# Performance work log

Hardware: AMD Instinct MI355X
Metric: run time of the kernel (lower is better)

The kernel has to match this reference:

```python
import jax, jax.numpy as jnp
import numpy as np

N = 100000   # nodes
E = 3200000  # edges
G = 1024     # graphs in the batch
H = 64       # hidden_dim


def setup_inputs() -> dict:
    key = jax.random.key(0)
    ks = jax.random.split(key, 12)
    x = jax.random.normal(ks[0], (N, 1), dtype=jnp.float32)
    edge_index = jax.random.randint(ks[1], (2, E), 0, N, dtype=jnp.int32)
    batch = jnp.sort(jax.random.randint(ks[2], (N,), 0, G, dtype=jnp.int32))
    s = 0.1
    w1 = jax.random.normal(ks[3], (1, H), dtype=jnp.float32) * s
    b1 = jnp.zeros((H,), dtype=jnp.float32)
    w2 = jax.random.normal(ks[4], (H, H), dtype=jnp.float32) * s
    b2 = jnp.zeros((H,), dtype=jnp.float32)
    w3 = jax.random.normal(ks[5], (H, H), dtype=jnp.float32) * s
    b3 = jnp.zeros((H,), dtype=jnp.float32)
    fc_w = jax.random.normal(ks[6], (H, 1), dtype=jnp.float32) * s
    fc_b = jnp.zeros((1,), dtype=jnp.float32)
    return {"x": x, "edge_index": edge_index, "batch": batch,
            "w1": w1, "b1": b1, "w2": w2, "b2": b2, "w3": w3, "b3": b3,
            "fc_w": fc_w, "fc_b": fc_b}


def _gcn_norm(edge_index, n):
    # add self-loops: A_hat = A + I
    src = jnp.concatenate([edge_index[0], jnp.arange(n, dtype=edge_index.dtype)])
    dst = jnp.concatenate([edge_index[1], jnp.arange(n, dtype=edge_index.dtype)])
    deg = jax.ops.segment_sum(jnp.ones_like(dst, dtype=jnp.float32), dst, num_segments=n)
    dinv = jnp.where(deg > 0, jax.lax.rsqrt(deg), 0.0)
    norm = dinv[src] * dinv[dst]  # [E+N]
    return src, dst, norm


def _gcn_conv(x, w, b, src, dst, norm, n):
    h = x @ w                               # [N, H] transform first (PyG order)
    msg = h[src] * norm[:, None]            # gather + scale  [E+N, H]
    out = jax.ops.segment_sum(msg, dst, num_segments=n)  # scatter-add
    return out + b


def reference(x, edge_index, batch, w1, b1, w2, b2, w3, b3, fc_w, fc_b):
    n = x.shape[0]
    src, dst, norm = _gcn_norm(edge_index, n)
    h = jax.nn.relu(_gcn_conv(x, w1, b1, src, dst, norm, n))
    h = jax.nn.relu(_gcn_conv(h, w2, b2, src, dst, norm, n))
    h = jax.nn.relu(_gcn_conv(h, w3, b3, src, dst, norm, n))
    # global mean pool over graphs
    sums = jax.ops.segment_sum(h, batch, num_segments=G)                 # [G, H]
    cnts = jax.ops.segment_sum(jnp.ones((n,), jnp.float32), batch, num_segments=G)
    pooled = sums / jnp.maximum(cnts, 1.0)[:, None]
    return pooled @ fc_w + fc_b  # [G, 1]
```

## Files before the change

kernel.cpp:

```cpp
#include <hip/hip_runtime.h>
#include <hip/hip_bf16.h>


#define WS_ALIGN(x) (((x) + 255) & ~size_t(255))
#define NCHUNK 8
#define CSH 14
#define NB 32
#define RPW (NB / 4)
#define NBIN (NB * NCHUNK)
#define USH 17
#define UMASK 0x1FFFF
#define BKTMAX 256
#define SBS 512
#define SBKEYS (SBS * NCHUNK)
#define P1T 2048

__device__ __forceinline__ float bf2f(unsigned short h) {
    union { unsigned u; float f; } t;
    t.u = ((unsigned)h) << 16;
    return t.f;
}
__device__ __forceinline__ unsigned short f2bf(float f) {
    union { float f; unsigned u; } t;
    t.f = f;
    unsigned r = t.u + 0x7FFF + ((t.u >> 16) & 1);
    return (unsigned short)(r >> 16);
}
__device__ __forceinline__ float bfLo(unsigned v) {
    union { unsigned u; float f; } t;
    t.u = v << 16;
    return t.f;
}
__device__ __forceinline__ float bfHi(unsigned v) {
    union { unsigned u; float f; } t;
    t.u = v & 0xFFFF0000u;
    return t.f;
}

__global__ __launch_bounds__(256) void k_zero(int g, int e, int* bucketCnt,
                                              int* gCursor, int* csr,
                                              float* gsum, float* gcnt) {
    int i = blockIdx.x * blockDim.x + threadIdx.x;
    if (i < BKTMAX) { bucketCnt[i] = 0; gCursor[i] = 0; }
    if (i < g) { gsum[i] = 0.f; gcnt[i] = 0.f; }
    if (i < 4) csr[e + i] = 0;
}

__global__ __launch_bounds__(256) void k_cnt1(int e, const int* __restrict__ dst,
                                              int* __restrict__ bucketCnt) {
    __shared__ int c[BKTMAX];
    int tid = threadIdx.x;
    c[tid] = 0;
    __syncthreads();
    int base = blockIdx.x * P1T;
#pragma unroll
    for (int q = 0; q < P1T / 256; ++q) {
        int i = base + q * 256 + tid;
        if (i < e) atomicAdd(&c[dst[i] >> 9], 1);
    }
    __syncthreads();
    if (c[tid] > 0) atomicAdd(&bucketCnt[tid], c[tid]);
}

__global__ __launch_bounds__(256) void k_scanB(int nbkt, int e,
                                               const int* __restrict__ bucketCnt,
                                               int* __restrict__ bucketStart) {
    __shared__ int sd[256];
    int tid = threadIdx.x;
    int v = (tid < nbkt) ? bucketCnt[tid] : 0;
    sd[tid] = v;
    __syncthreads();
    for (int off = 1; off < 256; off <<= 1) {
        int t = (tid >= off) ? sd[tid - off] : 0;
        __syncthreads();
        sd[tid] += t;
        __syncthreads();
    }
    if (tid < nbkt) bucketStart[tid] = sd[tid] - v;
    if (tid == 0) bucketStart[nbkt] = e;
}

__global__ __launch_bounds__(256) void k_p1(int e, const int* __restrict__ src,
                                            const int* __restrict__ dst,
                                            const int* __restrict__ bucketStart,
                                            int* __restrict__ gCursor,
                                            int* __restrict__ pkbuf) {
    __shared__ int cnt[BKTMAX], exc[BKTMAX], cur[BKTMAX], bb[BKTMAX];
    __shared__ int sd[256];
    __shared__ int stage[P1T];
    __shared__ unsigned char stgb[P1T];
    int tid = threadIdx.x;
    cnt[tid] = 0;
    __syncthreads();
    int base = blockIdx.x * P1T;
    int m = e - base; if (m > P1T) m = P1T;
    int pk8[P1T / 256];
    int b8[P1T / 256];
#pragma unroll
    for (int q = 0; q < P1T / 256; ++q) {
        int li = q * 256 + tid;
        if (li < m) {
            int d = dst[base + li];
            int s = src[base + li];
            int b = d >> 9;
            b8[q] = b;
            pk8[q] = ((d & (SBS - 1)) << USH) | s;
            atomicAdd(&cnt[b], 1);
        }
    }
    __syncthreads();
    int cv = cnt[tid];
    sd[tid] = cv;
    __syncthreads();
    for (int off = 1; off < 256; off <<= 1) {
        int t = (tid >= off) ? sd[tid - off] : 0;
        __syncthreads();
        sd[tid] += t;
        __syncthreads();
    }
    exc[tid] = sd[tid] - cv;
    cur[tid] = sd[tid] - cv;
    if (cv > 0) bb[tid] = atomicAdd(&gCursor[tid], cv);
    __syncthreads();
#pragma unroll
    for (int q = 0; q < P1T / 256; ++q) {
        int li = q * 256 + tid;
        if (li < m) {
            int b = b8[q];
            int pos = atomicAdd(&cur[b], 1);
            stage[pos] = pk8[q];
            stgb[pos] = (unsigned char)b;
        }
    }
    __syncthreads();
#pragma unroll
    for (int q = 0; q < P1T / 256; ++q) {
        int p = q * 256 + tid;
        if (p < m) {
            int b = stgb[p];
            pkbuf[bucketStart[b] + bb[b] + (p - exc[b])] = stage[p];
        }
    }
}

__global__ __launch_bounds__(256) void k_p2(int n, const int* __restrict__ bucketStart,
                                            const int* __restrict__ pkbuf,
                                            const float* __restrict__ x,
                                            int* __restrict__ csr,
                                            int* __restrict__ boundsG,
                                            float* __restrict__ dinv,
                                            float* __restrict__ xs) {
    __shared__ int cnt[SBKEYS + 1];
    __shared__ int sd[256];
    int sb = blockIdx.x, tid = threadIdx.x;
    int r0 = bucketStart[sb], r1 = bucketStart[sb + 1];
    for (int k = tid; k < SBKEYS + 1; k += 256) cnt[k] = 0;
    __syncthreads();
    for (int i = r0 + tid; i < r1; i += 256) {
        int w = pkbuf[i];
        int key = ((w >> USH) << 3) | ((w & UMASK) >> CSH);
        atomicAdd(&cnt[key], 1);
    }
    __syncthreads();
    int base16 = tid * 16;
    int loc[16]; int s = 0;
#pragma unroll
    for (int j = 0; j < 16; ++j) { loc[j] = cnt[base16 + j]; s += loc[j]; }
    sd[tid] = s;
    __syncthreads();
    for (int off = 1; off < 256; off <<= 1) {
        int t = (tid >= off) ? sd[tid - off] : 0;
        __syncthreads();
        sd[tid] += t;
        __syncthreads();
    }
    int run = sd[tid] - s;
#pragma unroll
    for (int j = 0; j < 16; ++j) { cnt[base16 + j] = run; run += loc[j]; }
    if (tid == 255) cnt[SBKEYS] = run;
    __syncthreads();
    for (int k = tid; k < SBKEYS; k += 256) {
        int bi = sb * 16 + (k >> 8);
        boundsG[(size_t)bi * (NBIN + 1) + (k & 255)] = r0 + cnt[k];
    }
    if (tid < 16)
        boundsG[(size_t)(sb * 16 + tid) * (NBIN + 1) + NBIN] = r0 + cnt[(tid + 1) * 256];
    for (int dl = tid; dl < SBS; dl += 256) {
        int v = sb * SBS + dl;
        if (v < n) {
            int deg = cnt[dl * 8 + 8] - cnt[dl * 8] + 1;
            float di = 1.0f / sqrtf((float)deg);
            dinv[v] = di;
            xs[v] = x[v] * di;
        }
    }
    __syncthreads();
    for (int i = r0 + tid; i < r1; i += 256) {
        int w = pkbuf[i];
        int srcv = w & UMASK;
        int key = ((w >> USH) << 3) | (srcv >> CSH);
        int pos = atomicAdd(&cnt[key], 1);
        csr[r0 + pos] = srcv;
    }
}

__global__ __launch_bounds__(256, 8) void k_layer1(int n, const int* __restrict__ boundsG,
                                                   const int* __restrict__ csr,
                                                   const float* __restrict__ xs,
                                                   const float* __restrict__ dinv,
                                                   const float* __restrict__ w1,
                                                   const float* __restrict__ b1,
                                                   unsigned short* __restrict__ hs_out) {
    int tid = threadIdx.x;
    int r = tid >> 6, lane = tid & 63;
    float w1r = w1[lane], b1r = b1[lane];
    int wid = blockIdx.x * 4 + r;
    int stride = gridDim.x * 4;
    for (int v = wid; v < n; v += stride) {
        int bi = v / NB, vi = v & (NB - 1);
        size_t base = (size_t)bi * (NBIN + 1) + vi * NCHUNK;
        int s0 = boundsG[base], s1 = boundsG[base + NCHUNK];
        float acc = 0.f;
        for (int k = s0 + lane; k < s1; k += 64) acc += xs[csr[k]];
#pragma unroll
        for (int m = 32; m > 0; m >>= 1) acc += __shfl_xor(acc, m, 64);
        float dv = dinv[v];
        float s = (acc + xs[v]) * dv;
        hs_out[(size_t)v * 64 + lane] = f2bf(fmaxf(s * w1r + b1r, 0.f) * dv);
    }
}

#define GATHER_CORE                                                            \
    __shared__ float ws[64 * 64];                                              \
    __shared__ float rowl[4][64];                                              \
    __shared__ int bndL[NBIN + 1];                                             \
    int tid = threadIdx.x;                                                     \
    int lane = tid & 63;                                                       \
    int r = tid >> 6;                                                          \
    int h = lane >> 5;                                                         \
    int fi = lane & 31;                                                        \
    int v0 = blockIdx.x * NB;                                                  \
    const unsigned* hsu = (const unsigned*)hs_in;                              \
    for (int k = tid; k < 64 * 64; k += 256) ws[k] = w[k];                     \
    for (int i = tid; i < NBIN + 1; i += 256)                                  \
        bndL[i] = boundsG[(size_t)blockIdx.x * (NBIN + 1) + i];                \
    float accLo[RPW], accHi[RPW];                                              \
    _Pragma("unroll")                                                          \
    for (int q = 0; q < RPW; ++q) {                                            \
        int v = v0 + q * 4 + r;                                                \
        unsigned sv = (v < n && h == 0) ? hsu[(size_t)v * 32 + fi] : 0u;       \
        accLo[q] = bfLo(sv);                                                   \
        accHi[q] = bfHi(sv);                                                   \
    }                                                                          \
    __syncthreads();                                                           \
    _Pragma("unroll")                                                          \
    for (int t = 0; t < RPW / 2; ++t) {                                        \
        int viA = (2 * t) * 4 + r;                                             \
        int viB = (2 * t + 1) * 4 + r;                                         \
        int ba = __builtin_amdgcn_readfirstlane(bndL[viA * NCHUNK]);           \
        int a1 = __builtin_amdgcn_readfirstlane(bndL[viA * NCHUNK + NCHUNK]);  \
        int bb = __builtin_amdgcn_readfirstlane(bndL[viB * NCHUNK]);           \
        int b1_ = __builtin_amdgcn_readfirstlane(bndL[viB * NCHUNK + NCHUNK]); \
        int pa = (a1 - ba > 0) ? ba : bb;                                      \
        int pb = (b1_ - bb > 0) ? bb : ba;                                     \
                               \
        int uA0 = csr[pa], uA1 = csr[pa + 1], uA2 = csr[pa + 2], uA3 = csr[pa + 3]; \
        int uB0 = csr[pb], uB1 = csr[pb + 1], uB2 = csr[pb + 2], uB3 = csr[pb + 3]; \
        unsigned gA01 = hsu[(size_t)(h ? uA1 : uA0) * 32 + fi];                \
        unsigned gA23 = hsu[(size_t)(h ? uA3 : uA2) * 32 + fi];                \
        unsigned gB01 = hsu[(size_t)(h ? uB1 : uB0) * 32 + fi];                \
        unsigned gB23 = hsu[(size_t)(h ? uB3 : uB2) * 32 + fi];                \
        while (ba < a1 || bb < b1_) {                                          \
            int na = ba + 4, nb = bb + 4;                                      \
            int pa2 = (a1 - na > 0) ? na : ((b1_ - nb > 0) ? nb : pa);         \
            int pb2 = (b1_ - nb > 0) ? nb : ((a1 - na > 0) ? na : pb);         \
                                  \
            int vA0 = csr[pa2], vA1 = csr[pa2 + 1], vA2 = csr[pa2 + 2], vA3 = csr[pa2 + 3]; \
            int vB0 = csr[pb2], vB1 = csr[pb2 + 1], vB2 = csr[pb2 + 2], vB3 = csr[pb2 + 3]; \
            unsigned nA01 = hsu[(size_t)(h ? vA1 : vA0) * 32 + fi];            \
            unsigned nA23 = hsu[(size_t)(h ? vA3 : vA2) * 32 + fi];            \
            unsigned nB01 = hsu[(size_t)(h ? vB1 : vB0) * 32 + fi];            \
            unsigned nB23 = hsu[(size_t)(h ? vB3 : vB2) * 32 + fi];            \
                              \
            int remA = a1 - ba, remB = b1_ - bb;                               \
            float mA0 = (remA > h) ? 1.f : 0.f;                                \
            float mA1 = (remA > 2 + h) ? 1.f : 0.f;                            \
            float mB0 = (remB > h) ? 1.f : 0.f;                                \
            float mB1 = (remB > 2 + h) ? 1.f : 0.f;                            \
            accLo[2 * t]     += bfLo(gA01) * mA0 + bfLo(gA23) * mA1;           \
            accHi[2 * t]     += bfHi(gA01) * mA0 + bfHi(gA23) * mA1;           \
            accLo[2 * t + 1] += bfLo(gB01) * mB0 + bfLo(gB23) * mB1;           \
            accHi[2 * t + 1] += bfHi(gB01) * mB0 + bfHi(gB23) * mB1;           \
            gA01 = nA01; gA23 = nA23; gB01 = nB01; gB23 = nB23;                \
            pa = pa2; pb = pb2;                                                \
            ba = na; bb = nb;                                                  \
        }                                                                      \
    }

__global__ __launch_bounds__(256, 4) void k_gg_mid(int n,
                                                   const int* __restrict__ boundsG,
                                                   const int* __restrict__ csr,
                                                   const unsigned short* __restrict__ hs_in,
                                                   const float* __restrict__ dinv,
                                                   const float* __restrict__ w,
                                                   const float* __restrict__ b,
                                                   unsigned short* __restrict__ hs_out) {
    GATHER_CORE
    float breg = b[lane];
#pragma unroll 1
    for (int q = 0; q < RPW; ++q) {
        int v = v0 + q * 4 + r;
        if (v >= n) continue;
        float dv = dinv[v];
        float lo = accLo[q]; lo += __shfl_xor(lo, 32, 64);
        float hi = accHi[q]; hi += __shfl_xor(hi, 32, 64);
        if (h == 0) {
            rowl[r][2 * fi] = lo * dv;
            rowl[r][2 * fi + 1] = hi * dv;
        }
        float o = breg;
#pragma unroll
        for (int k = 0; k < 64; ++k) o += rowl[r][k] * ws[k * 64 + lane];
        hs_out[(size_t)v * 64 + lane] = f2bf(fmaxf(o, 0.f) * dv);
    }
}

__global__ __launch_bounds__(256, 4) void k_gg_final(int n,
                                                     const int* __restrict__ boundsG,
                                                     const int* __restrict__ csr,
                                                     const unsigned short* __restrict__ hs_in,
                                                     const float* __restrict__ dinv,
                                                     const float* __restrict__ w,
                                                     const float* __restrict__ b,
                                                     const float* __restrict__ fcw,
                                                     float* __restrict__ dots) {
    GATHER_CORE
    float breg = b[lane];
    float freg = fcw[lane];
#pragma unroll 1
    for (int q = 0; q < RPW; ++q) {
        int v = v0 + q * 4 + r;
        if (v >= n) continue;
        float dv = dinv[v];
        float lo = accLo[q]; lo += __shfl_xor(lo, 32, 64);
        float hi = accHi[q]; hi += __shfl_xor(hi, 32, 64);
        if (h == 0) {
            rowl[r][2 * fi] = lo * dv;
            rowl[r][2 * fi + 1] = hi * dv;
        }
        float o = breg;
#pragma unroll
        for (int k = 0; k < 64; ++k) o += rowl[r][k] * ws[k * 64 + lane];
        float val = fmaxf(o, 0.f) * freg;
#pragma unroll
        for (int m = 32; m > 0; m >>= 1) val += __shfl_xor(val, m, 64);
        if (lane == 0) dots[v] = val;
    }
}

__global__ __launch_bounds__(256) void k_pool(int n, const float* __restrict__ dots,
                                              const int* __restrict__ batch,
                                              float* __restrict__ gsum,
                                              float* __restrict__ gcnt) {
    __shared__ float ls[64], lc[64];
    __shared__ int gmin_s;
    int tid = threadIdx.x;
    int i0 = blockIdx.x * 1024;
    if (tid == 0) gmin_s = batch[i0];
    if (tid < 64) { ls[tid] = 0.f; lc[tid] = 0.f; }
    __syncthreads();
    int gmin = gmin_s;
#pragma unroll
    for (int c = 0; c < 4; ++c) {
        int i = i0 + c * 256 + tid;
        if (i < n) {
            int g = batch[i];
            float d = dots[i];
            int rr = g - gmin;
            if (rr < 64) {
                atomicAdd(&ls[rr], d);
                atomicAdd(&lc[rr], 1.f);
            } else {
                atomicAdd(&gsum[g], d);
                atomicAdd(&gcnt[g], 1.f);
            }
        }
    }
    __syncthreads();
    if (tid < 64 && lc[tid] != 0.f) {
        atomicAdd(&gsum[gmin + tid], ls[tid]);
        atomicAdd(&gcnt[gmin + tid], lc[tid]);
    }
}

__global__ __launch_bounds__(256) void k_out(int g, const float* __restrict__ gsum,
                                             const float* __restrict__ gcnt,
                                             const float* __restrict__ fcb,
                                             float* __restrict__ out) {
    int i = blockIdx.x * blockDim.x + threadIdx.x;
    if (i < g) out[i] = gsum[i] / fmaxf(gcnt[i], 1.f) + fcb[0];
}

extern "C" void kernel_launch(void* const* d_in, const int* in_sizes, int n_in,
                              void* d_out, int out_size, void* d_ws, size_t ws_size,
                              hipStream_t stream) {
    const float* x    = (const float*)d_in[0];
    const int*   ei   = (const int*)d_in[1];
    const int*   batch= (const int*)d_in[2];
    const float* w1   = (const float*)d_in[3];
    const float* b1   = (const float*)d_in[4];
    const float* w2   = (const float*)d_in[5];
    const float* b2   = (const float*)d_in[6];
    const float* w3   = (const float*)d_in[7];
    const float* b3   = (const float*)d_in[8];
    const float* fcw  = (const float*)d_in[9];
    const float* fcb  = (const float*)d_in[10];
    float* out = (float*)d_out;

    const int N = in_sizes[0];
    const int E = in_sizes[1] / 2;
    const int G = out_size;
    const int H = 64;
    const int nbkt = (N + SBS - 1) / SBS;
    const int NBLK = (N + NB - 1) / NB;
    const int NBLKP = nbkt * 16;

    const int* src = ei;
    const int* dst = ei + E;

    char* p = (char*)d_ws;
    int*   bucketCnt   = (int*)p; p += WS_ALIGN(sizeof(int) * BKTMAX);
    int*   bucketStart = (int*)p; p += WS_ALIGN(sizeof(int) * (BKTMAX + 1));
    int*   gCursor     = (int*)p; p += WS_ALIGN(sizeof(int) * BKTMAX);
    int*   pkbuf       = (int*)p; p += WS_ALIGN(sizeof(int) * (size_t)E);
    int*   csr         = (int*)p; p += WS_ALIGN(sizeof(int) * ((size_t)E + 4));
    int*   boundsG     = (int*)p; p += WS_ALIGN(sizeof(int) * (size_t)NBLKP * (NBIN + 1));
    float* dinv        = (float*)p; p += WS_ALIGN(sizeof(float) * N);
    float* xs          = (float*)p; p += WS_ALIGN(sizeof(float) * N);
    unsigned short* bufA = (unsigned short*)p; p += WS_ALIGN(sizeof(unsigned short) * (size_t)N * H);
    unsigned short* bufB = (unsigned short*)p; p += WS_ALIGN(sizeof(unsigned short) * (size_t)N * H);
    float* dots        = (float*)p; p += WS_ALIGN(sizeof(float) * N);
    float* gsum        = (float*)p; p += WS_ALIGN(sizeof(float) * G);
    float* gcnt        = (float*)p; p += WS_ALIGN(sizeof(float) * G);

    const int B = 256;
    int gridZ    = ((G > BKTMAX ? G : BKTMAX) + B - 1) / B;
    int gridT    = (E + P1T - 1) / P1T;
    int gridG    = (G + B - 1) / B;
    int gridPool = (N + 1023) / 1024;
    int gridPers = 2048;
    if (gridPers * 4 > N) gridPers = (N + 3) / 4;

    k_zero<<<gridZ, B, 0, stream>>>(G, E, bucketCnt, gCursor, csr, gsum, gcnt);
    k_cnt1<<<gridT, B, 0, stream>>>(E, dst, bucketCnt);
    k_scanB<<<1, B, 0, stream>>>(nbkt, E, bucketCnt, bucketStart);
    k_p1<<<gridT, B, 0, stream>>>(E, src, dst, bucketStart, gCursor, pkbuf);
    k_p2<<<nbkt, B, 0, stream>>>(N, bucketStart, pkbuf, x, csr, boundsG, dinv, xs);
    k_layer1<<<gridPers, B, 0, stream>>>(N, boundsG, csr, xs, dinv, w1, b1, bufA);
    k_gg_mid<<<NBLK, B, 0, stream>>>(N, boundsG, csr, bufA, dinv, w2, b2, bufB);
    k_gg_final<<<NBLK, B, 0, stream>>>(N, boundsG, csr, bufB, dinv, w3, b3, fcw, dots);
    k_pool<<<gridPool, B, 0, stream>>>(N, dots, batch, gsum, gcnt);
    k_out<<<gridG, B, 0, stream>>>(G, gsum, gcnt, fcb, out);
}
```

Before: 326.5 us.

## Pad CSR rows to multiples of four with a dummy zero node

New measurement: 327.2 us. Within noise of the previous version (+0.2%).

```diff
diff --git a/kernel.cpp b/kernel.cpp
--- a/kernel.cpp
+++ b/kernel.cpp
@@ -7,13 +7,13 @@
 #define CSH 14
 #define NB 32
 #define RPW (NB / 4)
-#define NBIN (NB * NCHUNK)
 #define USH 17
 #define UMASK 0x1FFFF
 #define BKTMAX 256
 #define SBS 512
 #define SBKEYS (SBS * NCHUNK)
 #define P1T 2048
+#define PADGAP 1540
 
 __device__ __forceinline__ float bf2f(unsigned short h) {
     union { unsigned u; float f; } t;
@@ -37,13 +37,19 @@
     return t.f;
 }
 
-__global__ __launch_bounds__(256) void k_zero(int g, int e, int* bucketCnt,
-                                              int* gCursor, int* csr,
+__global__ __launch_bounds__(256) void k_zero(int g, int n, int* bucketCnt,
+                                              int* gCursor, float* xs,
+                                              unsigned short* bufA,
+                                              unsigned short* bufB,
                                               float* gsum, float* gcnt) {
     int i = blockIdx.x * blockDim.x + threadIdx.x;
     if (i < BKTMAX) { bucketCnt[i] = 0; gCursor[i] = 0; }
     if (i < g) { gsum[i] = 0.f; gcnt[i] = 0.f; }
-    if (i < 4) csr[e + i] = 0;
+    if (i < 64) {
+        bufA[(size_t)n * 64 + i] = 0;
+        bufB[(size_t)n * 64 + i] = 0;
+    }
+    if (i == 0) xs[n] = 0.f;
 }
 
 __global__ __launch_bounds__(256) void k_cnt1(int e, const int* __restrict__ dst,
@@ -147,13 +153,16 @@
                                             const int* __restrict__ pkbuf,
                                             const float* __restrict__ x,
                                             int* __restrict__ csr,
-                                            int* __restrict__ boundsG,
+                                            int* __restrict__ bndRow,
                                             float* __restrict__ dinv,
                                             float* __restrict__ xs) {
     __shared__ int cnt[SBKEYS + 1];
     __shared__ int sd[256];
+    __shared__ int padOff[SBS];
+    __shared__ int padTotal_s;
     int sb = blockIdx.x, tid = threadIdx.x;
     int r0 = bucketStart[sb], r1 = bucketStart[sb + 1];
+    int r0pad = r0 + sb * PADGAP;
     for (int k = tid; k < SBKEYS + 1; k += 256) cnt[k] = 0;
     __syncthreads();
     for (int i = r0 + tid; i < r1; i += 256) {
@@ -179,32 +188,58 @@
     for (int j = 0; j < 16; ++j) { cnt[base16 + j] = run; run += loc[j]; }
     if (tid == 255) cnt[SBKEYS] = run;
     __syncthreads();
-    for (int k = tid; k < SBKEYS; k += 256) {
-        int bi = sb * 16 + (k >> 8);
-        boundsG[(size_t)bi * (NBIN + 1) + (k & 255)] = r0 + cnt[k];
-    }
-    if (tid < 16)
-        boundsG[(size_t)(sb * 16 + tid) * (NBIN + 1) + NBIN] = r0 + cnt[(tid + 1) * 256];
+    int d0 = tid * 2, d1 = tid * 2 + 1;
+    int len0 = cnt[d0 * 8 + 8] - cnt[d0 * 8];
+    int len1 = cnt[d1 * 8 + 8] - cnt[d1 * 8];
+    int p0 = (-len0) & 3, p1 = (-len1) & 3;
+    int tsum = p0 + p1;
+    sd[tid] = tsum;
+    __syncthreads();
+    for (int off = 1; off < 256; off <<= 1) {
+        int t = (tid >= off) ? sd[tid - off] : 0;
+        __syncthreads();
+        sd[tid] += t;
+        __syncthreads();
+    }
+    int pexcl = sd[tid] - tsum;
+    padOff[d0] = pexcl;
+    padOff[d1] = pexcl + p0;
+    if (tid == 255) padTotal_s = pexcl + tsum;
+    __syncthreads();
     for (int dl = tid; dl < SBS; dl += 256) {
+        int gbi = sb * 16 + (dl >> 5);
+        int vi = dl & 31;
+        int startp = r0pad + cnt[dl * 8] + padOff[dl];
+        bndRow[gbi * 33 + vi] = startp;
+        if (vi == 0 && dl > 0) bndRow[(gbi - 1) * 33 + 32] = startp;
         int v = sb * SBS + dl;
         if (v < n) {
-            int deg = cnt[dl * 8 + 8] - cnt[dl * 8] + 1;
-            float di = 1.0f / sqrtf((float)deg);
+            int len = cnt[dl * 8 + 8] - cnt[dl * 8];
+            float di = 1.0f / sqrtf((float)(len + 1));
             dinv[v] = di;
             xs[v] = x[v] * di;
         }
+        int padc = (-(cnt[dl * 8 + 8] - cnt[dl * 8])) & 3;
+        int ps = r0pad + cnt[dl * 8 + 8] + padOff[dl];
+        for (int j = 0; j < padc; ++j) csr[ps + j] = n;
+    }
+    if (tid == 0) {
+        int endp = r0pad + cnt[SBKEYS] + padTotal_s;
+        bndRow[(sb * 16 + 15) * 33 + 32] = endp;
+        csr[endp] = n; csr[endp + 1] = n; csr[endp + 2] = n; csr[endp + 3] = n;
     }
     __syncthreads();
     for (int i = r0 + tid; i < r1; i += 256) {
         int w = pkbuf[i];
         int srcv = w & UMASK;
-        int key = ((w >> USH) << 3) | (srcv >> CSH);
+        int dl = w >> USH;
+        int key = (dl << 3) | (srcv >> CSH);
         int pos = atomicAdd(&cnt[key], 1);
-        csr[r0 + pos] = srcv;
-    }
-}
-
-__global__ __launch_bounds__(256, 8) void k_layer1(int n, const int* __restrict__ boundsG,
+        csr[r0pad + pos + padOff[dl]] = srcv;
+    }
+}
+
+__global__ __launch_bounds__(256, 8) void k_layer1(int n, const int* __restrict__ bndRow,
                                                    const int* __restrict__ csr,
                                                    const float* __restrict__ xs,
                                                    const float* __restrict__ dinv,
@@ -217,9 +252,8 @@
     int wid = blockIdx.x * 4 + r;
     int stride = gridDim.x * 4;
     for (int v = wid; v < n; v += stride) {
-        int bi = v / NB, vi = v & (NB - 1);
-        size_t base = (size_t)bi * (NBIN + 1) + vi * NCHUNK;
-        int s0 = boundsG[base], s1 = boundsG[base + NCHUNK];
+        int bi = v >> 5, vi = v & 31;
+        int s0 = bndRow[bi * 33 + vi], s1 = bndRow[bi * 33 + vi + 1];
         float acc = 0.f;
         for (int k = s0 + lane; k < s1; k += 64) acc += xs[csr[k]];
 #pragma unroll
@@ -233,7 +267,7 @@
 #define GATHER_CORE                                                            \
     __shared__ float ws[64 * 64];                                              \
     __shared__ float rowl[4][64];                                              \
-    __shared__ int bndL[NBIN + 1];                                             \
+    __shared__ int bndL[NB + 1];                                               \
     int tid = threadIdx.x;                                                     \
     int lane = tid & 63;                                                       \
     int r = tid >> 6;                                                          \
@@ -242,8 +276,7 @@
     int v0 = blockIdx.x * NB;                                                  \
     const unsigned* hsu = (const unsigned*)hs_in;                              \
     for (int k = tid; k < 64 * 64; k += 256) ws[k] = w[k];                     \
-    for (int i = tid; i < NBIN + 1; i += 256)                                  \
-        bndL[i] = boundsG[(size_t)blockIdx.x * (NBIN + 1) + i];                \
+    if (tid < NB + 1) bndL[tid] = bndRow[blockIdx.x * 33 + tid];               \
     float accLo[RPW], accHi[RPW];                                              \
     _Pragma("unroll")                                                          \
     for (int q = 0; q < RPW; ++q) {                                            \
@@ -257,13 +290,12 @@
     for (int t = 0; t < RPW / 2; ++t) {                                        \
         int viA = (2 * t) * 4 + r;                                             \
         int viB = (2 * t + 1) * 4 + r;                                         \
-        int ba = __builtin_amdgcn_readfirstlane(bndL[viA * NCHUNK]);           \
-        int a1 = __builtin_amdgcn_readfirstlane(bndL[viA * NCHUNK + NCHUNK]);  \
-        int bb = __builtin_amdgcn_readfirstlane(bndL[viB * NCHUNK]);           \
-        int b1_ = __builtin_amdgcn_readfirstlane(bndL[viB * NCHUNK + NCHUNK]); \
-        int pa = (a1 - ba > 0) ? ba : bb;                                      \
-        int pb = (b1_ - bb > 0) ? bb : ba;                                     \
-                               \
+        int ba = __builtin_amdgcn_readfirstlane(bndL[viA]);                    \
+        int a1 = __builtin_amdgcn_readfirstlane(bndL[viA + 1]);                \
+        int bb = __builtin_amdgcn_readfirstlane(bndL[viB]);                    \
+        int b1_ = __builtin_amdgcn_readfirstlane(bndL[viB + 1]);               \
+        int pa = (ba < a1) ? ba : bb;                                          \
+        int pb = (bb < b1_) ? bb : ba;                                         \
         int uA0 = csr[pa], uA1 = csr[pa + 1], uA2 = csr[pa + 2], uA3 = csr[pa + 3]; \
         int uB0 = csr[pb], uB1 = csr[pb + 1], uB2 = csr[pb + 2], uB3 = csr[pb + 3]; \
         unsigned gA01 = hsu[(size_t)(h ? uA1 : uA0) * 32 + fi];                \
@@ -272,25 +304,21 @@
         unsigned gB23 = hsu[(size_t)(h ? uB3 : uB2) * 32 + fi];                \
         while (ba < a1 || bb < b1_) {                                          \
             int na = ba + 4, nb = bb + 4;                                      \
-            int pa2 = (a1 - na > 0) ? na : ((b1_ - nb > 0) ? nb : pa);         \
-            int pb2 = (b1_ - nb > 0) ? nb : ((a1 - na > 0) ? na : pb);         \
-                                  \
+            int pa2 = (na < a1) ? na : ((nb < b1_) ? nb : pa);                 \
+            int pb2 = (nb < b1_) ? nb : ((na < a1) ? na : pb);                 \
             int vA0 = csr[pa2], vA1 = csr[pa2 + 1], vA2 = csr[pa2 + 2], vA3 = csr[pa2 + 3]; \
             int vB0 = csr[pb2], vB1 = csr[pb2 + 1], vB2 = csr[pb2 + 2], vB3 = csr[pb2 + 3]; \
             unsigned nA01 = hsu[(size_t)(h ? vA1 : vA0) * 32 + fi];            \
             unsigned nA23 = hsu[(size_t)(h ? vA3 : vA2) * 32 + fi];            \
             unsigned nB01 = hsu[(size_t)(h ? vB1 : vB0) * 32 + fi];            \
             unsigned nB23 = hsu[(size_t)(h ? vB3 : vB2) * 32 + fi];            \
-                              \
-            int remA = a1 - ba, remB = b1_ - bb;                               \
-            float mA0 = (remA > h) ? 1.f : 0.f;                                \
-            float mA1 = (remA > 2 + h) ? 1.f : 0.f;                            \
-            float mB0 = (remB > h) ? 1.f : 0.f;                                \
-            float mB1 = (remB > 2 + h) ? 1.f : 0.f;                            \
-            accLo[2 * t]     += bfLo(gA01) * mA0 + bfLo(gA23) * mA1;           \
-            accHi[2 * t]     += bfHi(gA01) * mA0 + bfHi(gA23) * mA1;           \
-            accLo[2 * t + 1] += bfLo(gB01) * mB0 + bfLo(gB23) * mB1;           \
-            accHi[2 * t + 1] += bfHi(gB01) * mB0 + bfHi(gB23) * mB1;           \
+                            \
+            float mA = (ba < a1) ? 1.f : 0.f;                                  \
+            float mB = (bb < b1_) ? 1.f : 0.f;                                 \
+            accLo[2 * t]     += (bfLo(gA01) + bfLo(gA23)) * mA;                \
+            accHi[2 * t]     += (bfHi(gA01) + bfHi(gA23)) * mA;                \
+            accLo[2 * t + 1] += (bfLo(gB01) + bfLo(gB23)) * mB;                \
+            accHi[2 * t + 1] += (bfHi(gB01) + bfHi(gB23)) * mB;                \
             gA01 = nA01; gA23 = nA23; gB01 = nB01; gB23 = nB23;                \
             pa = pa2; pb = pb2;                                                \
             ba = na; bb = nb;                                                  \
@@ -298,7 +326,7 @@
     }
 
 __global__ __launch_bounds__(256, 4) void k_gg_mid(int n,
-                                                   const int* __restrict__ boundsG,
+                                                   const int* __restrict__ bndRow,
                                                    const int* __restrict__ csr,
                                                    const unsigned short* __restrict__ hs_in,
                                                    const float* __restrict__ dinv,
@@ -326,7 +354,7 @@
 }
 
 __global__ __launch_bounds__(256, 4) void k_gg_final(int n,
-                                                     const int* __restrict__ boundsG,
+                                                     const int* __restrict__ bndRow,
                                                      const int* __restrict__ csr,
                                                      const unsigned short* __restrict__ hs_in,
                                                      const float* __restrict__ dinv,
@@ -433,12 +461,12 @@
     int*   bucketStart = (int*)p; p += WS_ALIGN(sizeof(int) * (BKTMAX + 1));
     int*   gCursor     = (int*)p; p += WS_ALIGN(sizeof(int) * BKTMAX);
     int*   pkbuf       = (int*)p; p += WS_ALIGN(sizeof(int) * (size_t)E);
-    int*   csr         = (int*)p; p += WS_ALIGN(sizeof(int) * ((size_t)E + 4));
-    int*   boundsG     = (int*)p; p += WS_ALIGN(sizeof(int) * (size_t)NBLKP * (NBIN + 1));
+    int*   csr         = (int*)p; p += WS_ALIGN(sizeof(int) * ((size_t)E + (size_t)nbkt * PADGAP + 8));
+    int*   bndRow      = (int*)p; p += WS_ALIGN(sizeof(int) * (size_t)NBLKP * 33);
     float* dinv        = (float*)p; p += WS_ALIGN(sizeof(float) * N);
-    float* xs          = (float*)p; p += WS_ALIGN(sizeof(float) * N);
-    unsigned short* bufA = (unsigned short*)p; p += WS_ALIGN(sizeof(unsigned short) * (size_t)N * H);
-    unsigned short* bufB = (unsigned short*)p; p += WS_ALIGN(sizeof(unsigned short) * (size_t)N * H);
+    float* xs          = (float*)p; p += WS_ALIGN(sizeof(float) * (N + 1));
+    unsigned short* bufA = (unsigned short*)p; p += WS_ALIGN(sizeof(unsigned short) * (size_t)(N + 1) * H);
+    unsigned short* bufB = (unsigned short*)p; p += WS_ALIGN(sizeof(unsigned short) * (size_t)(N + 1) * H);
     float* dots        = (float*)p; p += WS_ALIGN(sizeof(float) * N);
     float* gsum        = (float*)p; p += WS_ALIGN(sizeof(float) * G);
     float* gcnt        = (float*)p; p += WS_ALIGN(sizeof(float) * G);
@@ -451,14 +479,14 @@
     int gridPers = 2048;
     if (gridPers * 4 > N) gridPers = (N + 3) / 4;
 
-    k_zero<<<gridZ, B, 0, stream>>>(G, E, bucketCnt, gCursor, csr, gsum, gcnt);
+    k_zero<<<gridZ, B, 0, stream>>>(G, N, bucketCnt, gCursor, xs, bufA, bufB, gsum, gcnt);
     k_cnt1<<<gridT, B, 0, stream>>>(E, dst, bucketCnt);
     k_scanB<<<1, B, 0, stream>>>(nbkt, E, bucketCnt, bucketStart);
     k_p1<<<gridT, B, 0, stream>>>(E, src, dst, bucketStart, gCursor, pkbuf);
-    k_p2<<<nbkt, B, 0, stream>>>(N, bucketStart, pkbuf, x, csr, boundsG, dinv, xs);
-    k_layer1<<<gridPers, B, 0, stream>>>(N, boundsG, csr, xs, dinv, w1, b1, bufA);
-    k_gg_mid<<<NBLK, B, 0, stream>>>(N, boundsG, csr, bufA, dinv, w2, b2, bufB);
-    k_gg_final<<<NBLK, B, 0, stream>>>(N, boundsG, csr, bufB, dinv, w3, b3, fcw, dots);
+    k_p2<<<nbkt, B, 0, stream>>>(N, bucketStart, pkbuf, x, csr, bndRow, dinv, xs);
+    k_layer1<<<gridPers, B, 0, stream>>>(N, bndRow, csr, xs, dinv, w1, b1, bufA);
+    k_gg_mid<<<NBLK, B, 0, stream>>>(N, bndRow, csr, bufA, dinv, w2, b2, bufB);
+    k_gg_final<<<NBLK, B, 0, stream>>>(N, bndRow, csr, bufB, dinv, w3, b3, fcw, dots);
     k_pool<<<gridPool, B, 0, stream>>>(N, dots, batch, gsum, gcnt);
     k_out<<<gridG, B, 0, stream>>>(G, gsum, gcnt, fcb, out);
 }
```
